# Kernel tuning notes

Hardware: AMD Instinct MI355X
Metric: run time of the kernel (lower is better)

## Reference

```python
import jax, jax.numpy as jnp
import numpy as np

B, T, IN, H, L, C = 128, 256, 512, 512, 2, 64


def _lstm_layer(x, W_ih, W_hh, b_ih, b_hh):
    # x: [B, T, in]; W_ih: [4H, in]; W_hh: [4H, H]; PyTorch gate order i,f,g,o
    nH = W_hh.shape[1]
    x_proj = jnp.einsum('bti,gi->btg', x, W_ih) + b_ih + b_hh  # [B, T, 4H]

    def step(carry, xt):
        h, c = carry
        gates = xt + h @ W_hh.T
        i, f, g, o = jnp.split(gates, 4, axis=-1)
        i = jax.nn.sigmoid(i)
        f = jax.nn.sigmoid(f)
        g = jnp.tanh(g)
        o = jax.nn.sigmoid(o)
        c = f * c + i * g
        h = o * jnp.tanh(c)
        return (h, c), h

    h0 = jnp.zeros((x.shape[0], nH), x.dtype)
    _, hs = jax.lax.scan(step, (h0, h0), jnp.swapaxes(x_proj, 0, 1))
    return jnp.swapaxes(hs, 0, 1)  # [B, T, H]


def setup_inputs() -> dict:
    key = jax.random.key(0)
    ks = jax.random.split(key, 12)
    s_in = 1.0 / np.sqrt(H)
    inp = {
        'x': jax.random.normal(ks[0], (B, T, IN), dtype=jnp.float32),
        'y': jax.random.uniform(ks[1], (B, T - 1, C), dtype=jnp.float32),
        'batch_size': B,
        'W_ih0': jax.random.uniform(ks[2], (4 * H, IN), jnp.float32, -s_in, s_in),
        'W_hh0': jax.random.uniform(ks[3], (4 * H, H), jnp.float32, -s_in, s_in),
        'b_ih0': jax.random.uniform(ks[4], (4 * H,), jnp.float32, -s_in, s_in),
        'b_hh0': jax.random.uniform(ks[5], (4 * H,), jnp.float32, -s_in, s_in),
        'W_ih1': jax.random.uniform(ks[6], (4 * H, H), jnp.float32, -s_in, s_in),
        'W_hh1': jax.random.uniform(ks[7], (4 * H, H), jnp.float32, -s_in, s_in),
        'b_ih1': jax.random.uniform(ks[8], (4 * H,), jnp.float32, -s_in, s_in),
        'b_hh1': jax.random.uniform(ks[9], (4 * H,), jnp.float32, -s_in, s_in),
        'W_lin': jax.random.uniform(ks[10], (C, H), jnp.float32, -s_in, s_in),
        'b_lin': jax.random.uniform(ks[11], (C,), jnp.float32, -s_in, s_in),
    }
    return inp


def reference(x, y, batch_size, W_ih0, W_hh0, b_ih0, b_hh0,
              W_ih1, W_hh1, b_ih1, b_hh1, W_lin, b_lin):
    # stacked 2-layer LSTM (zero-initialized hidden state), dropout=0
    h = _lstm_layer(x, W_ih0, W_hh0, b_ih0, b_hh0)
    h = _lstm_layer(h, W_ih1, W_hh1, b_ih1, b_hh1)
    logits = jnp.einsum('bth,ch->btc', h[:, :-1, :], W_lin) + b_lin
    return jax.nn.sigmoid(logits)  # [B, T-1, C]
```

## Files before the change

### kernel.cpp

```cpp
#include <hip/hip_runtime.h>
#include <cstdint>
#include <cstddef>

#define B_  128
#define T_  256
#define IN_ 512
#define H_  512
#define C_  64
#define G4  2048

typedef __attribute__((ext_vector_type(8))) short short8;
typedef __attribute__((ext_vector_type(8))) __bf16 bf16x8_t;
typedef __attribute__((ext_vector_type(4))) float f32x4;

__device__ __forceinline__ float sigm(float x) { return 1.f / (1.f + __expf(-x)); }
__device__ __forceinline__ float tanh_f(float x) {
    float e = __expf(2.f * x);
    return 1.f - 2.f / (e + 1.f);
}
__device__ __forceinline__ unsigned short f2bf(float f) {
    unsigned u = __float_as_uint(f);
    u = (u + 0x7fffu + ((u >> 16) & 1u)) >> 16;
    return (unsigned short)u;
}
__device__ __forceinline__ float bf2f(unsigned short s) {
    return __uint_as_float(((unsigned)s) << 16);
}
__device__ __forceinline__ bf16x8_t as_bf(short8 s) {
    union { short8 s; bf16x8_t b; } u; u.s = s; return u.b;
}

#define SWZ(r, k) ((k) ^ (((r) & 7) << 3))

__global__ __launch_bounds__(256) void prep_w(
    const float* __restrict__ Wih, const float* __restrict__ Whh,
    const float* __restrict__ bih, const float* __restrict__ bhh,
    short* __restrict__ Whi, short* __restrict__ Wlo, float* __restrict__ bc)
{
    int idx = blockIdx.x * 256 + threadIdx.x;
    if (idx >= G4 * 1024) return;
    int jp = idx >> 10, k = idx & 1023;
    int u = jp >> 2, g = jp & 3;
    int src = g * H_ + u;
    float v = (k < IN_) ? Wih[(size_t)src * IN_ + k]
                        : Whh[(size_t)src * H_ + (k - IN_)];
    unsigned short hb = f2bf(v);
    Whi[idx] = (short)hb;
    Wlo[idx] = (short)f2bf(v - bf2f(hb));
    if (k == 0) bc[jp] = bih[src] + bhh[src];
}

__global__ __launch_bounds__(256) void lstm_step_mfma(
    const float* __restrict__ x,
    short* __restrict__ h0h, short* __restrict__ h0l,
    short* __restrict__ h1h, short* __restrict__ h1l,
    float* __restrict__ c0, float* __restrict__ c1,
    const short* __restrict__ W0h, const short* __restrict__ W0l,
    const short* __restrict__ W1h, const short* __restrict__ W1l,
    const float* __restrict__ bc0, const float* __restrict__ bc1,
    int kstep)
{
    const int wg = blockIdx.x;
    const int xcd = wg & 7, within = wg >> 3;
    const int layer = xcd >> 2;
    const int nt = (xcd & 3) * 16 + (within & 15);
    const int mt = within >> 4;
    const int t = kstep - layer;
    if (t < 0 || t >= T_) return;

    const int n0 = nt * 32;
    const int b0 = mt * 32;

    const short* Wh = layer ? W1h : W0h;
    const short* Wl = layer ? W1l : W0l;
    const float* bcp = layer ? bc1 : bc0;
    float* cst = layer ? c1 : c0;

    __shared__ short Ah[32][64], Al[32][64];
    __shared__ short Bh[32][64], Bl[32][64];
    __shared__ float Gs[32][33];

    const int tid = threadIdx.x;
    const int lane = tid & 63;
    const int wv = tid >> 6;
    const int mr = (wv & 1) * 16;
    const int nc = (wv >> 1) * 16;
    const int lr = lane & 15;
    const int kg = (lane >> 4) * 8;

    const int srow = tid >> 3;
    const int skq = (tid & 7) * 8;
    const int bg_s = b0 + srow;

    f32x4 acc = {0.f, 0.f, 0.f, 0.f};
    const int kmax = (t == 0) ? IN_ : 1024;

    for (int k0 = 0; k0 < kmax; k0 += 64) {
        const int kk = k0 + skq;
        short8 ahi, alo;
        if (layer == 0 && kk < IN_) {
            const float* xr = x + ((size_t)bg_s * T_ + t) * IN_ + kk;
            float4 f0 = *(const float4*)xr;
            float4 f1 = *(const float4*)(xr + 4);
            float vv[8] = {f0.x, f0.y, f0.z, f0.w, f1.x, f1.y, f1.z, f1.w};
            #pragma unroll
            for (int j = 0; j < 8; ++j) {
                unsigned short hb = f2bf(vv[j]);
                ahi[j] = (short)hb;
                alo[j] = (short)f2bf(vv[j] - bf2f(hb));
            }
        } else {
            const short *sh, *sl;
            size_t off;
            if (kk < IN_) {
                off = ((size_t)bg_s * T_ + t) * H_ + kk;
                sh = h0h; sl = h0l;
            } else {
                off = ((size_t)bg_s * T_ + (t - 1)) * H_ + (kk - IN_);
                sh = layer ? h1h : h0h;
                sl = layer ? h1l : h0l;
            }
            ahi = *(const short8*)(sh + off);
            alo = *(const short8*)(sl + off);
        }
        const size_t woff = (size_t)(n0 + srow) * 1024 + kk;
        short8 bhi = *(const short8*)(Wh + woff);
        short8 blo = *(const short8*)(Wl + woff);

        __syncthreads();
        *(short8*)&Ah[srow][SWZ(srow, skq)] = ahi;
        *(short8*)&Al[srow][SWZ(srow, skq)] = alo;
        *(short8*)&Bh[srow][SWZ(srow, skq)] = bhi;
        *(short8*)&Bl[srow][SWZ(srow, skq)] = blo;
        __syncthreads();

        #pragma unroll
        for (int ks = 0; ks < 2; ++ks) {
            const int kb = ks * 32 + kg;
            short8 a_h = *(const short8*)&Ah[mr + lr][SWZ(mr + lr, kb)];
            short8 a_l = *(const short8*)&Al[mr + lr][SWZ(mr + lr, kb)];
            short8 b_h = *(const short8*)&Bh[nc + lr][SWZ(nc + lr, kb)];
            short8 b_l = *(const short8*)&Bl[nc + lr][SWZ(nc + lr, kb)];
            acc = __builtin_amdgcn_mfma_f32_16x16x32_bf16(as_bf(a_h), as_bf(b_h), acc, 0, 0, 0);
            acc = __builtin_amdgcn_mfma_f32_16x16x32_bf16(as_bf(a_h), as_bf(b_l), acc, 0, 0, 0);
            acc = __builtin_amdgcn_mfma_f32_16x16x32_bf16(as_bf(a_l), as_bf(b_h), acc, 0, 0, 0);
        }
    }

    __syncthreads();
    #pragma unroll
    for (int j = 0; j < 4; ++j)
        Gs[mr + (lane >> 4) * 4 + j][nc + lr] = acc[j];
    __syncthreads();

    const int r = tid >> 3, u = tid & 7;
    const int bg = b0 + r;
    const int ug = (n0 >> 2) + u;
    const float gi = Gs[r][4 * u + 0] + bcp[n0 + 4 * u + 0];
    const float gf = Gs[r][4 * u + 1] + bcp[n0 + 4 * u + 1];
    const float gg = Gs[r][4 * u + 2] + bcp[n0 + 4 * u + 2];
    const float go = Gs[r][4 * u + 3] + bcp[n0 + 4 * u + 3];
    const float i_ = sigm(gi), f_ = sigm(gf), g_ = tanh_f(gg), o_ = sigm(go);
    const float cold = (t > 0) ? cst[bg * H_ + ug] : 0.f;
    const float cn = f_ * cold + i_ * g_;
    const float hn = o_ * tanh_f(cn);
    cst[bg * H_ + ug] = cn;
    short* hh = layer ? h1h : h0h;
    short* hl = layer ? h1l : h0l;
    const unsigned short hb = f2bf(hn);
    hh[((size_t)bg * T_ + t) * H_ + ug] = (short)hb;
    hl[((size_t)bg * T_ + t) * H_ + ug] = (short)f2bf(hn - bf2f(hb));
}

__global__ __launch_bounds__(256) void linear_sig(
    const short* __restrict__ hh, const short* __restrict__ hl,
    const float* __restrict__ Wl, const float* __restrict__ bl,
    float* __restrict__ out)
{
    __shared__ float Ast[32][68];
    __shared__ float Bst[32][68];

    const int tid = threadIdx.x;
    const int tx = tid & 15, ty = tid >> 4;
    const int m0 = blockIdx.x * 64;

    float acc[4][4] = {};

    const int lr = tid >> 2;
    const int lk = (tid & 3) << 3;
    const int m = m0 + lr;
    const int b = m / 255, tt = m % 255;
    const size_t hbase = ((size_t)b * T_ + tt) * H_;
    const float* wrow = Wl + (size_t)lr * 512;

    for (int k0 = 0; k0 < 512; k0 += 32) {
        short8 h8 = *(const short8*)(hh + hbase + k0 + lk);
        short8 l8 = *(const short8*)(hl + hbase + k0 + lk);
        float av[8];
        #pragma unroll
        for (int j = 0; j < 8; ++j)
            av[j] = bf2f((unsigned short)h8[j]) + bf2f((unsigned short)l8[j]);
        float4 w0 = *(const float4*)(wrow + k0 + lk);
        float4 w1 = *(const float4*)(wrow + k0 + lk + 4);
        __syncthreads();
        #pragma unroll
        for (int j = 0; j < 8; ++j) Ast[lk + j][lr] = av[j];
        Bst[lk + 0][lr] = w0.x; Bst[lk + 1][lr] = w0.y;
        Bst[lk + 2][lr] = w0.z; Bst[lk + 3][lr] = w0.w;
        Bst[lk + 4][lr] = w1.x; Bst[lk + 5][lr] = w1.y;
        Bst[lk + 6][lr] = w1.z; Bst[lk + 7][lr] = w1.w;
        __syncthreads();
        #pragma unroll
        for (int k = 0; k < 32; ++k) {
            float4 av4 = *(const float4*)&Ast[k][4 * ty];
            float4 wv4 = *(const float4*)&Bst[k][4 * tx];
            float ar[4] = {av4.x, av4.y, av4.z, av4.w};
            float wr[4] = {wv4.x, wv4.y, wv4.z, wv4.w};
            #pragma unroll
            for (int i = 0; i < 4; ++i)
                #pragma unroll
                for (int j = 0; j < 4; ++j)
                    acc[i][j] += ar[i] * wr[j];
        }
    }

    const float4 blv = *(const float4*)&bl[4 * tx];
    const float blr[4] = {blv.x, blv.y, blv.z, blv.w};
    #pragma unroll
    for (int i = 0; i < 4; ++i) {
        const int mg = m0 + 4 * ty + i;
        float4 o;
        o.x = sigm(acc[i][0] + blr[0]);
        o.y = sigm(acc[i][1] + blr[1]);
        o.z = sigm(acc[i][2] + blr[2]);
        o.w = sigm(acc[i][3] + blr[3]);
        *(float4*)&out[(size_t)mg * C_ + 4 * tx] = o;
    }
}

extern "C" void kernel_launch(void* const* d_in, const int* in_sizes, int n_in,
                              void* d_out, int out_size, void* d_ws, size_t ws_size,
                              hipStream_t stream)
{
    (void)in_sizes; (void)n_in; (void)out_size; (void)ws_size;

    const float* x    = (const float*)d_in[0];
    const float* Wih0 = (const float*)d_in[3];
    const float* Whh0 = (const float*)d_in[4];
    const float* bih0 = (const float*)d_in[5];
    const float* bhh0 = (const float*)d_in[6];
    const float* Wih1 = (const float*)d_in[7];
    const float* Whh1 = (const float*)d_in[8];
    const float* bih1 = (const float*)d_in[9];
    const float* bhh1 = (const float*)d_in[10];
    const float* Wlin = (const float*)d_in[11];
    const float* blin = (const float*)d_in[12];
    float* out = (float*)d_out;

    char* p = (char*)d_ws;
    auto carve = [&](size_t bytes) { char* r = p; p += (bytes + 255) & ~(size_t)255; return r; };
    short* W0h = (short*)carve((size_t)G4 * 1024 * 2);
    short* W0l = (short*)carve((size_t)G4 * 1024 * 2);
    short* W1h = (short*)carve((size_t)G4 * 1024 * 2);
    short* W1l = (short*)carve((size_t)G4 * 1024 * 2);
    float* bc0 = (float*)carve(G4 * 4);
    float* bc1 = (float*)carve(G4 * 4);
    float* c0  = (float*)carve((size_t)B_ * H_ * 4);
    float* c1  = (float*)carve((size_t)B_ * H_ * 4);
    short* h0h = (short*)carve((size_t)B_ * T_ * H_ * 2);
    short* h0l = (short*)carve((size_t)B_ * T_ * H_ * 2);
    short* h1h = (short*)carve((size_t)B_ * T_ * H_ * 2);
    short* h1l = (short*)carve((size_t)B_ * T_ * H_ * 2);

    prep_w<<<8192, 256, 0, stream>>>(Wih0, Whh0, bih0, bhh0, W0h, W0l, bc0);
    prep_w<<<8192, 256, 0, stream>>>(Wih1, Whh1, bih1, bhh1, W1h, W1l, bc1);

    for (int k = 0; k <= T_; ++k)
        lstm_step_mfma<<<512, 256, 0, stream>>>(x, h0h, h0l, h1h, h1l, c0, c1,
                                                W0h, W0l, W1h, W1l, bc0, bc1, k);

    linear_sig<<<510, 256, 0, stream>>>(h1h, h1l, Wlin, blin, out);
}
```

Measured before the change: 4.299 ms.

## Stage full weight slice in LDS, preconvert x, and double-buffer hidden states

Each per-timestep workgroup now loads its whole 32x1024 weight slice (hi and lo) into LDS once and runs 64 batch rows with 512 threads. It reads A operands directly from global memory with no per-chunk barriers. The input x is split into bf16 hi/lo once in a separate kernel rather than at every step. Layer-0 h and the h1 low part move to two-slot ping-pong buffers, and the final linear layer reads only the bf16 high part of h1. The aim is to cut per-step barrier and conversion overhead and memory footprint, at the cost of more LDS per block (about 136KB), fewer blocks, and slightly lower precision in the output projection.

```diff
diff --git a/kernel.cpp b/kernel.cpp
--- a/kernel.cpp
+++ b/kernel.cpp
@@ -50,130 +50,163 @@
     if (k == 0) bc[jp] = bih[src] + bhh[src];
 }
 
-__global__ __launch_bounds__(256) void lstm_step_mfma(
-    const float* __restrict__ x,
+__global__ __launch_bounds__(256) void prep_x(
+    const float* __restrict__ x, short* __restrict__ xh, short* __restrict__ xl)
+{
+    int idx = blockIdx.x * 256 + threadIdx.x;
+    if (idx >= (B_ * T_ * IN_) / 8) return;
+    const size_t base = (size_t)idx * 8;
+    float4 f0 = *(const float4*)(x + base);
+    float4 f1 = *(const float4*)(x + base + 4);
+    float vv[8] = {f0.x, f0.y, f0.z, f0.w, f1.x, f1.y, f1.z, f1.w};
+    short8 h8, l8;
+    #pragma unroll
+    for (int j = 0; j < 8; ++j) {
+        unsigned short hb = f2bf(vv[j]);
+        h8[j] = (short)hb;
+        l8[j] = (short)f2bf(vv[j] - bf2f(hb));
+    }
+    *(short8*)(xh + base) = h8;
+    *(short8*)(xl + base) = l8;
+}
+
+__global__ __launch_bounds__(512, 2) void lstm_step_p(
+    const short* __restrict__ xh, const short* __restrict__ xl,
     short* __restrict__ h0h, short* __restrict__ h0l,
-    short* __restrict__ h1h, short* __restrict__ h1l,
+    short* __restrict__ h1l,
+    short* __restrict__ h1h,
     float* __restrict__ c0, float* __restrict__ c1,
     const short* __restrict__ W0h, const short* __restrict__ W0l,
     const short* __restrict__ W1h, const short* __restrict__ W1l,
     const float* __restrict__ bc0, const float* __restrict__ bc1,
     int kstep)
 {
+    __shared__ short WldsH[32][1024];
+    __shared__ short WldsL[32][1024];
+    __shared__ float Gs[64][33];
+
     const int wg = blockIdx.x;
-    const int xcd = wg & 7, within = wg >> 3;
+    const int xcd = wg & 7;
+    const int within = wg >> 3;
     const int layer = xcd >> 2;
     const int nt = (xcd & 3) * 16 + (within & 15);
-    const int mt = within >> 4;
+    const int mh = within >> 4;
     const int t = kstep - layer;
     if (t < 0 || t >= T_) return;
 
     const int n0 = nt * 32;
-    const int b0 = mt * 32;
-
-    const short* Wh = layer ? W1h : W0h;
-    const short* Wl = layer ? W1l : W0l;
+    const int b0 = mh * 64;
+
+    const short* Wgh = layer ? W1h : W0h;
+    const short* Wgl = layer ? W1l : W0l;
     const float* bcp = layer ? bc1 : bc0;
     float* cst = layer ? c1 : c0;
 
-    __shared__ short Ah[32][64], Al[32][64];
-    __shared__ short Bh[32][64], Bl[32][64];
-    __shared__ float Gs[32][33];
-
     const int tid = threadIdx.x;
+
+    {
+        const int row = tid >> 4;
+        const int kb16 = (tid & 15) * 64;
+        const short* gh = Wgh + (size_t)(n0 + row) * 1024 + kb16;
+        const short* gl = Wgl + (size_t)(n0 + row) * 1024 + kb16;
+        #pragma unroll
+        for (int j = 0; j < 8; ++j) {
+            short8 vh = *(const short8*)(gh + j * 8);
+            short8 vl = *(const short8*)(gl + j * 8);
+            *(short8*)&WldsH[row][SWZ(row, kb16 + j * 8)] = vh;
+            *(short8*)&WldsL[row][SWZ(row, kb16 + j * 8)] = vl;
+        }
+    }
+
+    const int r_up = tid >> 3;
+    const int u_up = tid & 7;
+    const float4 bq = *(const float4*)&bcp[n0 + 4 * u_up];
+    __syncthreads();
+
     const int lane = tid & 63;
-    const int wv = tid >> 6;
-    const int mr = (wv & 1) * 16;
-    const int nc = (wv >> 1) * 16;
+    const int wid = tid >> 6;
+    const int mq = wid & 3;
+    const int nq = wid >> 2;
     const int lr = lane & 15;
-    const int kg = (lane >> 4) * 8;
-
-    const int srow = tid >> 3;
-    const int skq = (tid & 7) * 8;
-    const int bg_s = b0 + srow;
+    const int koff = (lane >> 4) * 8;
+    const int b_lane = b0 + mq * 16 + lr;
+    const int colr = nq * 16 + lr;
 
     f32x4 acc = {0.f, 0.f, 0.f, 0.f};
-    const int kmax = (t == 0) ? IN_ : 1024;
-
-    for (int k0 = 0; k0 < kmax; k0 += 64) {
-        const int kk = k0 + skq;
-        short8 ahi, alo;
-        if (layer == 0 && kk < IN_) {
-            const float* xr = x + ((size_t)bg_s * T_ + t) * IN_ + kk;
-            float4 f0 = *(const float4*)xr;
-            float4 f1 = *(const float4*)(xr + 4);
-            float vv[8] = {f0.x, f0.y, f0.z, f0.w, f1.x, f1.y, f1.z, f1.w};
-            #pragma unroll
-            for (int j = 0; j < 8; ++j) {
-                unsigned short hb = f2bf(vv[j]);
-                ahi[j] = (short)hb;
-                alo[j] = (short)f2bf(vv[j] - bf2f(hb));
-            }
+
+    {
+        const short *ih, *il;
+        if (layer == 0) {
+            const size_t o = ((size_t)b_lane * T_ + t) * 512 + koff;
+            ih = xh + o; il = xl + o;
         } else {
-            const short *sh, *sl;
-            size_t off;
-            if (kk < IN_) {
-                off = ((size_t)bg_s * T_ + t) * H_ + kk;
-                sh = h0h; sl = h0l;
-            } else {
-                off = ((size_t)bg_s * T_ + (t - 1)) * H_ + (kk - IN_);
-                sh = layer ? h1h : h0h;
-                sl = layer ? h1l : h0l;
-            }
-            ahi = *(const short8*)(sh + off);
-            alo = *(const short8*)(sl + off);
-        }
-        const size_t woff = (size_t)(n0 + srow) * 1024 + kk;
-        short8 bhi = *(const short8*)(Wh + woff);
-        short8 blo = *(const short8*)(Wl + woff);
-
-        __syncthreads();
-        *(short8*)&Ah[srow][SWZ(srow, skq)] = ahi;
-        *(short8*)&Al[srow][SWZ(srow, skq)] = alo;
-        *(short8*)&Bh[srow][SWZ(srow, skq)] = bhi;
-        *(short8*)&Bl[srow][SWZ(srow, skq)] = blo;
-        __syncthreads();
-
-        #pragma unroll
-        for (int ks = 0; ks < 2; ++ks) {
-            const int kb = ks * 32 + kg;
-            short8 a_h = *(const short8*)&Ah[mr + lr][SWZ(mr + lr, kb)];
-            short8 a_l = *(const short8*)&Al[mr + lr][SWZ(mr + lr, kb)];
-            short8 b_h = *(const short8*)&Bh[nc + lr][SWZ(nc + lr, kb)];
-            short8 b_l = *(const short8*)&Bl[nc + lr][SWZ(nc + lr, kb)];
-            acc = __builtin_amdgcn_mfma_f32_16x16x32_bf16(as_bf(a_h), as_bf(b_h), acc, 0, 0, 0);
-            acc = __builtin_amdgcn_mfma_f32_16x16x32_bf16(as_bf(a_h), as_bf(b_l), acc, 0, 0, 0);
-            acc = __builtin_amdgcn_mfma_f32_16x16x32_bf16(as_bf(a_l), as_bf(b_h), acc, 0, 0, 0);
-        }
-    }
-
-    __syncthreads();
+            const size_t o = ((size_t)(t & 1) * B_ + b_lane) * 512 + koff;
+            ih = h0h + o; il = h0l + o;
+        }
+        #pragma unroll 4
+        for (int kc = 0; kc < 16; ++kc) {
+            short8 ah = *(const short8*)(ih + kc * 32);
+            short8 al = *(const short8*)(il + kc * 32);
+            const int kg = kc * 32 + koff;
+            short8 bh = *(const short8*)&WldsH[colr][SWZ(colr, kg)];
+            short8 bl = *(const short8*)&WldsL[colr][SWZ(colr, kg)];
+            acc = __builtin_amdgcn_mfma_f32_16x16x32_bf16(as_bf(ah), as_bf(bh), acc, 0, 0, 0);
+            acc = __builtin_amdgcn_mfma_f32_16x16x32_bf16(as_bf(ah), as_bf(bl), acc, 0, 0, 0);
+            acc = __builtin_amdgcn_mfma_f32_16x16x32_bf16(as_bf(al), as_bf(bh), acc, 0, 0, 0);
+        }
+    }
+    if (t > 0) {
+        const short *rh, *rl;
+        if (layer == 0) {
+            const size_t o = ((size_t)((t - 1) & 1) * B_ + b_lane) * 512 + koff;
+            rh = h0h + o; rl = h0l + o;
+        } else {
+            rh = h1h + ((size_t)b_lane * T_ + (t - 1)) * 512 + koff;
+            rl = h1l + ((size_t)((t - 1) & 1) * B_ + b_lane) * 512 + koff;
+        }
+        #pragma unroll 4
+        for (int kc = 0; kc < 16; ++kc) {
+            short8 ah = *(const short8*)(rh + kc * 32);
+            short8 al = *(const short8*)(rl + kc * 32);
+            const int kg = 512 + kc * 32 + koff;
+            short8 bh = *(const short8*)&WldsH[colr][SWZ(colr, kg)];
+            short8 bl = *(const short8*)&WldsL[colr][SWZ(colr, kg)];
+            acc = __builtin_amdgcn_mfma_f32_16x16x32_bf16(as_bf(ah), as_bf(bh), acc, 0, 0, 0);
+            acc = __builtin_amdgcn_mfma_f32_16x16x32_bf16(as_bf(ah), as_bf(bl), acc, 0, 0, 0);
+            acc = __builtin_amdgcn_mfma_f32_16x16x32_bf16(as_bf(al), as_bf(bh), acc, 0, 0, 0);
+        }
+    }
+
     #pragma unroll
     for (int j = 0; j < 4; ++j)
-        Gs[mr + (lane >> 4) * 4 + j][nc + lr] = acc[j];
+        Gs[mq * 16 + (lane >> 4) * 4 + j][nq * 16 + lr] = acc[j];
     __syncthreads();
 
-    const int r = tid >> 3, u = tid & 7;
-    const int bg = b0 + r;
-    const int ug = (n0 >> 2) + u;
-    const float gi = Gs[r][4 * u + 0] + bcp[n0 + 4 * u + 0];
-    const float gf = Gs[r][4 * u + 1] + bcp[n0 + 4 * u + 1];
-    const float gg = Gs[r][4 * u + 2] + bcp[n0 + 4 * u + 2];
-    const float go = Gs[r][4 * u + 3] + bcp[n0 + 4 * u + 3];
+    const float gi = Gs[r_up][4 * u_up + 0] + bq.x;
+    const float gf = Gs[r_up][4 * u_up + 1] + bq.y;
+    const float gg = Gs[r_up][4 * u_up + 2] + bq.z;
+    const float go = Gs[r_up][4 * u_up + 3] + bq.w;
     const float i_ = sigm(gi), f_ = sigm(gf), g_ = tanh_f(gg), o_ = sigm(go);
+    const int bg = b0 + r_up;
+    const int ug = nt * 8 + u_up;
     const float cold = (t > 0) ? cst[bg * H_ + ug] : 0.f;
     const float cn = f_ * cold + i_ * g_;
     const float hn = o_ * tanh_f(cn);
     cst[bg * H_ + ug] = cn;
-    short* hh = layer ? h1h : h0h;
-    short* hl = layer ? h1l : h0l;
     const unsigned short hb = f2bf(hn);
-    hh[((size_t)bg * T_ + t) * H_ + ug] = (short)hb;
-    hl[((size_t)bg * T_ + t) * H_ + ug] = (short)f2bf(hn - bf2f(hb));
+    const unsigned short lb = f2bf(hn - bf2f(hb));
+    if (layer == 0) {
+        const size_t o = ((size_t)(t & 1) * B_ + bg) * 512 + ug;
+        h0h[o] = (short)hb;
+        h0l[o] = (short)lb;
+    } else {
+        h1h[((size_t)bg * T_ + t) * 512 + ug] = (short)hb;
+        h1l[((size_t)(t & 1) * B_ + bg) * 512 + ug] = (short)lb;
+    }
 }
 
 __global__ __launch_bounds__(256) void linear_sig(
-    const short* __restrict__ hh, const short* __restrict__ hl,
+    const short* __restrict__ hh,
     const float* __restrict__ Wl, const float* __restrict__ bl,
     float* __restrict__ out)
 {
@@ -195,25 +228,20 @@
 
     for (int k0 = 0; k0 < 512; k0 += 32) {
         short8 h8 = *(const short8*)(hh + hbase + k0 + lk);
-        short8 l8 = *(const short8*)(hl + hbase + k0 + lk);
-        float av[8];
-        #pragma unroll
-        for (int j = 0; j < 8; ++j)
-            av[j] = bf2f((unsigned short)h8[j]) + bf2f((unsigned short)l8[j]);
         float4 w0 = *(const float4*)(wrow + k0 + lk);
         float4 w1 = *(const float4*)(wrow + k0 + lk + 4);
         __syncthreads();
         #pragma unroll
-        for (int j = 0; j < 8; ++j) Ast[lk + j][lr] = av[j];
+        for (int j = 0; j < 8; ++j) Ast[lk + j][lr] = bf2f((unsigned short)h8[j]);
         Bst[lk + 0][lr] = w0.x; Bst[lk + 1][lr] = w0.y;
         Bst[lk + 2][lr] = w0.z; Bst[lk + 3][lr] = w0.w;
         Bst[lk + 4][lr] = w1.x; Bst[lk + 5][lr] = w1.y;
         Bst[lk + 6][lr] = w1.z; Bst[lk + 7][lr] = w1.w;
         __syncthreads();
         #pragma unroll
-        for (int k = 0; k < 32; ++k) {
-            float4 av4 = *(const float4*)&Ast[k][4 * ty];
-            float4 wv4 = *(const float4*)&Bst[k][4 * tx];
+        for (int kk = 0; kk < 32; ++kk) {
+            float4 av4 = *(const float4*)&Ast[kk][4 * ty];
+            float4 wv4 = *(const float4*)&Bst[kk][4 * tx];
             float ar[4] = {av4.x, av4.y, av4.z, av4.w};
             float wr[4] = {wv4.x, wv4.y, wv4.z, wv4.w};
             #pragma unroll
@@ -267,17 +295,21 @@
     float* bc1 = (float*)carve(G4 * 4);
     float* c0  = (float*)carve((size_t)B_ * H_ * 4);
     float* c1  = (float*)carve((size_t)B_ * H_ * 4);
-    short* h0h = (short*)carve((size_t)B_ * T_ * H_ * 2);
-    short* h0l = (short*)carve((size_t)B_ * T_ * H_ * 2);
+    short* xh  = (short*)carve((size_t)B_ * T_ * IN_ * 2);
+    short* xl  = (short*)carve((size_t)B_ * T_ * IN_ * 2);
+    short* h0h = (short*)carve((size_t)2 * B_ * H_ * 2);
+    short* h0l = (short*)carve((size_t)2 * B_ * H_ * 2);
+    short* h1l = (short*)carve((size_t)2 * B_ * H_ * 2);
     short* h1h = (short*)carve((size_t)B_ * T_ * H_ * 2);
-    short* h1l = (short*)carve((size_t)B_ * T_ * H_ * 2);
 
     prep_w<<<8192, 256, 0, stream>>>(Wih0, Whh0, bih0, bhh0, W0h, W0l, bc0);
     prep_w<<<8192, 256, 0, stream>>>(Wih1, Whh1, bih1, bhh1, W1h, W1l, bc1);
+    prep_x<<<8192, 256, 0, stream>>>(x, xh, xl);
 
     for (int k = 0; k <= T_; ++k)
-        lstm_step_mfma<<<512, 256, 0, stream>>>(x, h0h, h0l, h1h, h1l, c0, c1,
-                                                W0h, W0l, W1h, W1l, bc0, bc1, k);
-
-    linear_sig<<<510, 256, 0, stream>>>(h1h, h1l, Wlin, blin, out);
-}
+        lstm_step_p<<<256, 512, 0, stream>>>(xh, xl, h0h, h0l, h1l, h1h,
+                                             c0, c1, W0h, W0l, W1h, W1l,
+                                             bc0, bc1, k);
+
+    linear_sig<<<510, 256, 0, stream>>>(h1h, Wlin, blin, out);
+}
```

Result: slower. 5.679 ms (+32.1%).
